# Performance work log

Hardware: AMD Instinct MI355X
Metric: run time of the kernel (lower is better)

## Reference

```python
import jax, jax.numpy as jnp
import numpy as np

N_EMBED = 1024
N_HEADS = 16
CTX = 2048
B, T = 4, 2048
HD = N_EMBED // N_HEADS


def setup_inputs() -> dict:
    key = jax.random.key(0)
    ks = jax.random.split(key, 5)
    scale = 1.0 / np.sqrt(N_EMBED)
    return {
        "x": jax.random.normal(ks[0], (B, T, N_EMBED), dtype=jnp.float32),
        "wq": jax.random.normal(ks[1], (N_EMBED, N_EMBED), dtype=jnp.float32) * scale,
        "wk": jax.random.normal(ks[2], (N_EMBED, N_EMBED), dtype=jnp.float32) * scale,
        "wv": jax.random.normal(ks[3], (N_EMBED, N_EMBED), dtype=jnp.float32) * scale,
        "wo": jax.random.normal(ks[4], (N_EMBED, N_EMBED), dtype=jnp.float32) * scale,
    }


def reference(x, wq, wk, wv, wo):
    b, t, c = x.shape
    # nn.Linear applies x @ W.T ; split heads -> [B, H, T, hd]
    def proj(w):
        return jnp.einsum("btc,dc->btd", x, w).reshape(b, t, N_HEADS, HD).transpose(0, 2, 1, 3)
    q, k, v = proj(wq), proj(wk), proj(wv)
    scores = jnp.einsum("bhqd,bhkd->bhqk", q, k) * (HD ** -0.5)
    causal = jnp.tril(jnp.ones((t, t), dtype=bool))
    scores = jnp.where(causal[None, None, :, :], scores, -jnp.inf)
    a = jax.nn.softmax(scores, axis=-1)
    o = jnp.einsum("bhqk,bhkd->bhqd", a, v)  # [B,H,T,hd]
    o = o.transpose(0, 2, 1, 3).reshape(b, t, c)
    return jnp.einsum("btc,dc->btd", o, wo)
```

## Files before the change

kernel.cpp:

```cpp
#include <hip/hip_runtime.h>
#include <stdint.h>


typedef __attribute__((ext_vector_type(8))) short bf16x8;
typedef __attribute__((ext_vector_type(4))) float f32x4;
typedef unsigned short us;

#define LOG2E 1.4426950408889634f

#define GL2LDS16(g, l)                                                          \
  __builtin_amdgcn_global_load_lds(                                             \
      (const __attribute__((address_space(1))) unsigned int*)(g),               \
      (__attribute__((address_space(3))) unsigned int*)(l), 16, 0, 0)

__device__ inline us f2bf(float f) {
  union { float f; unsigned int u; } v; v.f = f;
  unsigned int u = v.u;
  u += 0x7FFFu + ((u >> 16) & 1u);
  return (us)(u >> 16);
}

__global__ void cast_all(const float* __restrict__ x,
                         const float* __restrict__ w0, const float* __restrict__ w1,
                         const float* __restrict__ w2, const float* __restrict__ w3,
                         us* __restrict__ xb, us* __restrict__ wbuf) {
  int i = (blockIdx.x * blockDim.x + threadIdx.x) * 8;
  const float* src;
  us* dst;
  float sc = 1.0f;
  if (i < (8 << 20)) {
    src = x + i; dst = xb + i;
  } else {
    int j = i - (8 << 20);
    int seg = j >> 20;
    int off = j & ((1 << 20) - 1);
    const float* w = (seg == 0) ? w0 : (seg == 1) ? w1 : (seg == 2) ? w2 : w3;
    if (seg == 0) sc = 0.125f * LOG2E;
    src = w + off; dst = wbuf + j;
  }
  float4 a = *reinterpret_cast<const float4*>(src);
  float4 b = *reinterpret_cast<const float4*>(src + 4);
  union { us u[8]; uint4 v; } o;
  o.u[0] = f2bf(a.x * sc); o.u[1] = f2bf(a.y * sc);
  o.u[2] = f2bf(a.z * sc); o.u[3] = f2bf(a.w * sc);
  o.u[4] = f2bf(b.x * sc); o.u[5] = f2bf(b.y * sc);
  o.u[6] = f2bf(b.z * sc); o.u[7] = f2bf(b.w * sc);
  *reinterpret_cast<uint4*>(dst) = o.v;
}

template <int OUT_BF16>
__global__ __launch_bounds__(256, 2) void gemm_bt(
    const us* __restrict__ A, const us* __restrict__ Bw,
    void* __restrict__ Cv, int M, int N, int K) {
  __shared__ __align__(16) us Al[128 * 32];
  __shared__ __align__(16) us Bl[128 * 32];
  const int tid = threadIdx.x;
  const int lane = tid & 63;
  const int w = tid >> 6;
  const int quad = lane >> 4;
  const int l16 = lane & 15;
  const int m0 = blockIdx.y * 128;
  const int n0 = blockIdx.x * 128;
  const int wm = w >> 1, wn = w & 1;
  const int arow = lane >> 2;
  const int acol = (lane & 3) * 8;
  f32x4 acc[4][4] = {};

  for (int k0 = 0; k0 < K; k0 += 32) {
    __syncthreads();
    for (int c = 0; c < 2; ++c) {
      int chunk = 2 * w + c;
      int ldsoff = __builtin_amdgcn_readfirstlane(chunk * 512);
      GL2LDS16(A + (size_t)(m0 + chunk * 16 + arow) * K + k0 + acol, &Al[ldsoff]);
      GL2LDS16(Bw + (size_t)(n0 + chunk * 16 + arow) * K + k0 + acol, &Bl[ldsoff]);
    }
    __syncthreads();
    bf16x8 af[4], bfr[4];
#pragma unroll
    for (int mi = 0; mi < 4; ++mi)
      af[mi] = *reinterpret_cast<const bf16x8*>(&Al[(wm * 64 + mi * 16 + l16) * 32 + quad * 8]);
#pragma unroll
    for (int ni = 0; ni < 4; ++ni)
      bfr[ni] = *reinterpret_cast<const bf16x8*>(&Bl[(wn * 64 + ni * 16 + l16) * 32 + quad * 8]);
#pragma unroll
    for (int mi = 0; mi < 4; ++mi)
#pragma unroll
      for (int ni = 0; ni < 4; ++ni)
        acc[mi][ni] = __builtin_amdgcn_mfma_f32_16x16x32_bf16(af[mi], bfr[ni], acc[mi][ni], 0, 0, 0);
  }

#pragma unroll
  for (int mi = 0; mi < 4; ++mi)
#pragma unroll
    for (int ni = 0; ni < 4; ++ni)
#pragma unroll
      for (int r = 0; r < 4; ++r) {
        int row = m0 + wm * 64 + mi * 16 + quad * 4 + r;
        int col = n0 + wn * 64 + ni * 16 + l16;
        if (OUT_BF16)
          ((us*)Cv)[(size_t)row * N + col] = f2bf(acc[mi][ni][r]);
        else
          ((float*)Cv)[(size_t)row * N + col] = acc[mi][ni][r];
      }
}

__global__ __launch_bounds__(256) void transpose_v(const us* __restrict__ QKV,
                                                   us* __restrict__ Vt) {
  __shared__ __align__(16) us lds[64 * 80];
  const int bid = blockIdx.x;
  const int kt = bid & 31;
  const int bh = bid >> 5;
  const int b = bh >> 4, h = bh & 15;
  const int tid = threadIdx.x;
#pragma unroll
  for (int it = 0; it < 2; ++it) {
    int u = it * 256 + tid;
    int j = u >> 3;
    int dc = (u & 7) * 8;
    uint4 raw = *reinterpret_cast<const uint4*>(
        &QKV[((size_t)(b * 2048 + kt * 64 + j)) * 3072 + 2048 + h * 64 + dc]);
    us tmp[8];
    *reinterpret_cast<uint4*>(tmp) = raw;
    int sj = (j & 15) * 4 + (j >> 4);
#pragma unroll
    for (int e = 0; e < 8; ++e) lds[(dc + e) * 80 + sj] = tmp[e];
  }
  __syncthreads();
  int d = tid >> 2, c = tid & 3;
  size_t orow = ((size_t)(bh * 64 + d)) * 2048 + kt * 64 + c * 16;
  *reinterpret_cast<uint4*>(&Vt[orow]) = *reinterpret_cast<const uint4*>(&lds[d * 80 + c * 16]);
  *reinterpret_cast<uint4*>(&Vt[orow + 8]) = *reinterpret_cast<const uint4*>(&lds[d * 80 + c * 16 + 8]);
}

__global__ __launch_bounds__(512, 4) void attn(
    const us* __restrict__ QKV, const us* __restrict__ Vt,
    us* __restrict__ O) {
  __shared__ __align__(16) us Kl[64 * 64];
  __shared__ __align__(16) us Vl[64 * 64];
  __shared__ __align__(16) us Pl[8][16 * 64];
  const int bid = blockIdx.x;
  const int pr = bid & 7;
  const int h = (bid >> 3) & 15;
  const int b = bid >> 7;
  const int q0A = pr * 128, q0B = (15 - pr) * 128;
  const int tid = threadIdx.x, lane = tid & 63, w = tid >> 6;
  const int quad = lane >> 4, l16 = lane & 15;
  const size_t rowbase = (size_t)b * 2048;
  const int qcol = h * 64;
  const int kcol = 1024 + h * 64;

  bf16x8 qfA[2], qfB[2];
#pragma unroll
  for (int dc = 0; dc < 2; ++dc) {
    qfA[dc] = *reinterpret_cast<const bf16x8*>(
        &QKV[(rowbase + q0A + w * 16 + l16) * 3072 + qcol + dc * 32 + quad * 8]);
    qfB[dc] = *reinterpret_cast<const bf16x8*>(
        &QKV[(rowbase + q0B + w * 16 + l16) * 3072 + qcol + dc * 32 + quad * 8]);
  }

  f32x4 oaccA[4] = {}, oaccB[4] = {};
  float lsumA[4] = {}, lsumB[4] = {};

  const int rr = tid >> 3;
  const int gu = (tid & 7) ^ (rr & 7);
  const int base = __builtin_amdgcn_readfirstlane(w * 512);
  const int nB = 2 * (15 - pr) + 2;

  auto process = [&](int q0, bf16x8 (&qf)[2], f32x4 (&oacc)[4],
                     float (&lsum)[4], int kt) {
    f32x4 s[4] = {};
#pragma unroll
    for (int t = 0; t < 4; ++t) {
      int krow = t * 16 + l16;
#pragma unroll
      for (int dc = 0; dc < 2; ++dc) {
        bf16x8 kf = *reinterpret_cast<const bf16x8*>(
            &Kl[krow * 64 + (((dc * 4 + quad) ^ (l16 & 7)) * 8)]);
        s[t] = __builtin_amdgcn_mfma_f32_16x16x32_bf16(qf[dc], kf, s[t], 0, 0, 0);
      }
    }
    float p[4][4];
    bool do_mask = (kt * 64 + 63) > (q0 + w * 16);
    if (do_mask) {
#pragma unroll
      for (int t = 0; t < 4; ++t)
#pragma unroll
        for (int r = 0; r < 4; ++r) {
          float e = exp2f(s[t][r]);
          int kg = kt * 64 + t * 16 + l16;
          int qgl = q0 + w * 16 + quad * 4 + r;
          p[t][r] = (kg <= qgl) ? e : 0.f;
          lsum[r] += p[t][r];
        }
    } else {
#pragma unroll
      for (int t = 0; t < 4; ++t)
#pragma unroll
        for (int r = 0; r < 4; ++r) {
          float e = exp2f(s[t][r]);
          p[t][r] = e;
          lsum[r] += e;
        }
    }
#pragma unroll
    for (int r = 0; r < 4; ++r) {
      int prow = quad * 4 + r;
      uint2 val;
      val.x = __builtin_amdgcn_perm(__float_as_uint(p[1][r]), __float_as_uint(p[0][r]), 0x07060302u);
      val.y = __builtin_amdgcn_perm(__float_as_uint(p[3][r]), __float_as_uint(p[2][r]), 0x07060302u);
      char* dst = (char*)&Pl[w][0] + prow * 128 +
                  (((l16 >> 1) ^ (prow & 7)) * 16) + (l16 & 1) * 8;
      *reinterpret_cast<uint2*>(dst) = val;
    }
    asm volatile("s_waitcnt lgkmcnt(0)" ::: "memory");
#pragma unroll
    for (int kc = 0; kc < 2; ++kc) {
      bf16x8 pf = *reinterpret_cast<const bf16x8*>(
          (const char*)&Pl[w][0] + l16 * 128 + (((kc * 4 + quad) ^ (l16 & 7)) * 16));
#pragma unroll
      for (int dt = 0; dt < 4; ++dt) {
        bf16x8 vf = *reinterpret_cast<const bf16x8*>(
            &Vl[(dt * 16 + l16) * 64 + (((kc * 4 + quad) ^ (l16 & 7)) * 8)]);
        oacc[dt] = __builtin_amdgcn_mfma_f32_16x16x32_bf16(pf, vf, oacc[dt], 0, 0, 0);
      }
    }
  };

  for (int kt = 0; kt < nB; ++kt) {
    __syncthreads();
    GL2LDS16(QKV + (rowbase + kt * 64 + rr) * 3072 + kcol + gu * 8, &Kl[base]);
    GL2LDS16(Vt + ((size_t)((b * 16 + h) * 64 + rr)) * 2048 + kt * 64 + gu * 8, &Vl[base]);
    __syncthreads();
    if (kt * 64 <= q0B + w * 16 + 15) process(q0B, qfB, oaccB, lsumB, kt);
    if (kt * 64 <= q0A + w * 16 + 15) process(q0A, qfA, oaccA, lsumA, kt);
  }

  auto finalize = [&](int q0, f32x4 (&oacc)[4], float (&lsum)[4]) {
    float inv[4];
#pragma unroll
    for (int r = 0; r < 4; ++r) {
      float v = lsum[r];
      v += __shfl_xor(v, 1); v += __shfl_xor(v, 2);
      v += __shfl_xor(v, 4); v += __shfl_xor(v, 8);
      inv[r] = 1.0f / v;
    }
#pragma unroll
    for (int dt = 0; dt < 4; ++dt)
#pragma unroll
      for (int r = 0; r < 4; ++r) {
        int row = q0 + w * 16 + quad * 4 + r;
        O[(rowbase + row) * 1024 + qcol + dt * 16 + l16] = f2bf(oacc[dt][r] * inv[r]);
      }
  };
  finalize(q0A, oaccA, lsumA);
  finalize(q0B, oaccB, lsumB);
}

extern "C" void kernel_launch(void* const* d_in, const int* in_sizes, int n_in,
                              void* d_out, int out_size, void* d_ws, size_t ws_size,
                              hipStream_t stream) {
  const float* x = (const float*)d_in[0];
  const float* wq = (const float*)d_in[1];
  const float* wk = (const float*)d_in[2];
  const float* wv = (const float*)d_in[3];
  const float* wo = (const float*)d_in[4];

  const int BT = 8192, E = 1024;
  const size_t NX = (size_t)BT * E;
  const size_t NW = (size_t)E * E;

  us* xb = (us*)d_ws;
  us* wbuf = xb + NX;
  us* QKV = wbuf + 4 * NW;
  us* VtB = QKV + (size_t)BT * 3 * E;
  us* Ob = xb;

  cast_all<<<(int)((NX + 4 * NW) / 8 / 256), 256, 0, stream>>>(x, wq, wk, wv, wo, xb, wbuf);

  gemm_bt<1><<<dim3(24, 64), 256, 0, stream>>>(xb, wbuf, QKV, BT, 3 * E, E);
  transpose_v<<<64 * 32, 256, 0, stream>>>(QKV, VtB);
  attn<<<4 * 16 * 8, 512, 0, stream>>>(QKV, VtB, Ob);
  gemm_bt<0><<<dim3(8, 64), 256, 0, stream>>>(Ob, wbuf + 3 * NW, (float*)d_out, BT, E, E);
}
```

Measured before the change: 261.7 us.

## Widen GEMM K-tile to 64 with swizzled LDS, compute softmax row sums via MFMA

The projection GEMM now stages 64-wide K tiles with an XOR-swizzled LDS layout, which halves the number of barrier pairs per K loop and avoids bank conflicts on fragment reads. The attention kernel drops per-element lsum adds and the shuffle reduction, and instead gets row sums from an extra MFMA of the bf16 P fragment against a ones vector. exp2f is replaced with the hardware exp2 builtin. The GEMM uses more LDS per block, and row sums are now taken from bf16-rounded P rather than fp32 values, which slightly changes the normalisation.

```diff
diff --git a/kernel.cpp b/kernel.cpp
--- a/kernel.cpp
+++ b/kernel.cpp
@@ -52,8 +52,8 @@
 __global__ __launch_bounds__(256, 2) void gemm_bt(
     const us* __restrict__ A, const us* __restrict__ Bw,
     void* __restrict__ Cv, int M, int N, int K) {
-  __shared__ __align__(16) us Al[128 * 32];
-  __shared__ __align__(16) us Bl[128 * 32];
+  __shared__ __align__(16) us Al[128 * 64];
+  __shared__ __align__(16) us Bl[128 * 64];
   const int tid = threadIdx.x;
   const int lane = tid & 63;
   const int w = tid >> 6;
@@ -62,31 +62,42 @@
   const int m0 = blockIdx.y * 128;
   const int n0 = blockIdx.x * 128;
   const int wm = w >> 1, wn = w & 1;
-  const int arow = lane >> 2;
-  const int acol = (lane & 3) * 8;
+  const int srow_base = w * 8 + (lane >> 3);
+  const int sunit = lane & 7;
   f32x4 acc[4][4] = {};
 
-  for (int k0 = 0; k0 < K; k0 += 32) {
-    __syncthreads();
-    for (int c = 0; c < 2; ++c) {
-      int chunk = 2 * w + c;
-      int ldsoff = __builtin_amdgcn_readfirstlane(chunk * 512);
-      GL2LDS16(A + (size_t)(m0 + chunk * 16 + arow) * K + k0 + acol, &Al[ldsoff]);
-      GL2LDS16(Bw + (size_t)(n0 + chunk * 16 + arow) * K + k0 + acol, &Bl[ldsoff]);
-    }
-    __syncthreads();
-    bf16x8 af[4], bfr[4];
-#pragma unroll
-    for (int mi = 0; mi < 4; ++mi)
-      af[mi] = *reinterpret_cast<const bf16x8*>(&Al[(wm * 64 + mi * 16 + l16) * 32 + quad * 8]);
-#pragma unroll
-    for (int ni = 0; ni < 4; ++ni)
-      bfr[ni] = *reinterpret_cast<const bf16x8*>(&Bl[(wn * 64 + ni * 16 + l16) * 32 + quad * 8]);
-#pragma unroll
-    for (int mi = 0; mi < 4; ++mi)
-#pragma unroll
-      for (int ni = 0; ni < 4; ++ni)
-        acc[mi][ni] = __builtin_amdgcn_mfma_f32_16x16x32_bf16(af[mi], bfr[ni], acc[mi][ni], 0, 0, 0);
+  for (int k0 = 0; k0 < K; k0 += 64) {
+    __syncthreads();
+#pragma unroll
+    for (int it = 0; it < 4; ++it) {
+      int row = it * 32 + srow_base;
+      int gu = sunit ^ (row & 7);
+      int base = __builtin_amdgcn_readfirstlane((it * 256 + w * 64) * 8);
+      GL2LDS16(A + (size_t)(m0 + row) * K + k0 + gu * 8, &Al[base]);
+      GL2LDS16(Bw + (size_t)(n0 + row) * K + k0 + gu * 8, &Bl[base]);
+    }
+    __syncthreads();
+#pragma unroll
+    for (int kk = 0; kk < 2; ++kk) {
+      bf16x8 af[4], bfr[4];
+#pragma unroll
+      for (int mi = 0; mi < 4; ++mi) {
+        int row = wm * 64 + mi * 16 + l16;
+        af[mi] = *reinterpret_cast<const bf16x8*>(
+            &Al[row * 64 + (((kk * 4 + quad) ^ (row & 7)) * 8)]);
+      }
+#pragma unroll
+      for (int ni = 0; ni < 4; ++ni) {
+        int row = wn * 64 + ni * 16 + l16;
+        bfr[ni] = *reinterpret_cast<const bf16x8*>(
+            &Bl[row * 64 + (((kk * 4 + quad) ^ (row & 7)) * 8)]);
+      }
+#pragma unroll
+      for (int mi = 0; mi < 4; ++mi)
+#pragma unroll
+        for (int ni = 0; ni < 4; ++ni)
+          acc[mi][ni] = __builtin_amdgcn_mfma_f32_16x16x32_bf16(af[mi], bfr[ni], acc[mi][ni], 0, 0, 0);
+    }
   }
 
 #pragma unroll
@@ -149,6 +160,9 @@
   const int qcol = h * 64;
   const int kcol = 1024 + h * 64;
 
+  const bf16x8 ones = {(short)0x3F80, (short)0x3F80, (short)0x3F80, (short)0x3F80,
+                       (short)0x3F80, (short)0x3F80, (short)0x3F80, (short)0x3F80};
+
   bf16x8 qfA[2], qfB[2];
 #pragma unroll
   for (int dc = 0; dc < 2; ++dc) {
@@ -159,7 +173,7 @@
   }
 
   f32x4 oaccA[4] = {}, oaccB[4] = {};
-  float lsumA[4] = {}, lsumB[4] = {};
+  f32x4 laccA = {}, laccB = {};
 
   const int rr = tid >> 3;
   const int gu = (tid & 7) ^ (rr & 7);
@@ -167,7 +181,7 @@
   const int nB = 2 * (15 - pr) + 2;
 
   auto process = [&](int q0, bf16x8 (&qf)[2], f32x4 (&oacc)[4],
-                     float (&lsum)[4], int kt) {
+                     f32x4& lacc, int kt) {
     f32x4 s[4] = {};
 #pragma unroll
     for (int t = 0; t < 4; ++t) {
@@ -186,21 +200,17 @@
       for (int t = 0; t < 4; ++t)
 #pragma unroll
         for (int r = 0; r < 4; ++r) {
-          float e = exp2f(s[t][r]);
+          float e = __builtin_amdgcn_exp2f(s[t][r]);
           int kg = kt * 64 + t * 16 + l16;
           int qgl = q0 + w * 16 + quad * 4 + r;
           p[t][r] = (kg <= qgl) ? e : 0.f;
-          lsum[r] += p[t][r];
         }
     } else {
 #pragma unroll
       for (int t = 0; t < 4; ++t)
 #pragma unroll
-        for (int r = 0; r < 4; ++r) {
-          float e = exp2f(s[t][r]);
-          p[t][r] = e;
-          lsum[r] += e;
-        }
+        for (int r = 0; r < 4; ++r)
+          p[t][r] = __builtin_amdgcn_exp2f(s[t][r]);
     }
 #pragma unroll
     for (int r = 0; r < 4; ++r) {
@@ -217,6 +227,7 @@
     for (int kc = 0; kc < 2; ++kc) {
       bf16x8 pf = *reinterpret_cast<const bf16x8*>(
           (const char*)&Pl[w][0] + l16 * 128 + (((kc * 4 + quad) ^ (l16 & 7)) * 16));
+      lacc = __builtin_amdgcn_mfma_f32_16x16x32_bf16(pf, ones, lacc, 0, 0, 0);
 #pragma unroll
       for (int dt = 0; dt < 4; ++dt) {
         bf16x8 vf = *reinterpret_cast<const bf16x8*>(
@@ -231,29 +242,21 @@
     GL2LDS16(QKV + (rowbase + kt * 64 + rr) * 3072 + kcol + gu * 8, &Kl[base]);
     GL2LDS16(Vt + ((size_t)((b * 16 + h) * 64 + rr)) * 2048 + kt * 64 + gu * 8, &Vl[base]);
     __syncthreads();
-    if (kt * 64 <= q0B + w * 16 + 15) process(q0B, qfB, oaccB, lsumB, kt);
-    if (kt * 64 <= q0A + w * 16 + 15) process(q0A, qfA, oaccA, lsumA, kt);
-  }
-
-  auto finalize = [&](int q0, f32x4 (&oacc)[4], float (&lsum)[4]) {
-    float inv[4];
-#pragma unroll
-    for (int r = 0; r < 4; ++r) {
-      float v = lsum[r];
-      v += __shfl_xor(v, 1); v += __shfl_xor(v, 2);
-      v += __shfl_xor(v, 4); v += __shfl_xor(v, 8);
-      inv[r] = 1.0f / v;
-    }
+    if (kt * 64 <= q0B + w * 16 + 15) process(q0B, qfB, oaccB, laccB, kt);
+    if (kt * 64 <= q0A + w * 16 + 15) process(q0A, qfA, oaccA, laccA, kt);
+  }
+
+  auto finalize = [&](int q0, f32x4 (&oacc)[4], f32x4& lacc) {
 #pragma unroll
     for (int dt = 0; dt < 4; ++dt)
 #pragma unroll
       for (int r = 0; r < 4; ++r) {
         int row = q0 + w * 16 + quad * 4 + r;
-        O[(rowbase + row) * 1024 + qcol + dt * 16 + l16] = f2bf(oacc[dt][r] * inv[r]);
+        O[(rowbase + row) * 1024 + qcol + dt * 16 + l16] = f2bf(oacc[dt][r] / lacc[r]);
       }
   };
-  finalize(q0A, oaccA, lsumA);
-  finalize(q0B, oaccB, lsumB);
+  finalize(q0A, oaccA, laccA);
+  finalize(q0B, oaccB, laccB);
 }
 
 extern "C" void kernel_launch(void* const* d_in, const int* in_sizes, int n_in,
```

After: 239.3 us. 1.09x faster.
